# Kernel tuning notes

Measured on AMD Instinct MI355X. Metric: run time of the kernel, lower is better.

The kernel has to match this reference:

```python
import jax, jax.numpy as jnp
import numpy as np
from math import sqrt

BS, SEQ, NV, DM, K = 16, 1024, 512, 256, 8
EPS = 0.05  # sinkhorn epsilon
TEMP = 0.07  # concrete-bernoulli temperature


def setup_inputs() -> dict:
    key = jax.random.key(0)
    k1, k2, k3 = jax.random.split(key, 3)
    x = jax.random.normal(k1, (BS, SEQ, NV), jnp.float32)
    # nn.Linear(seq_len, d_model): weight [d_model, seq_len], bias [d_model]
    W = jax.random.normal(k2, (DM, SEQ), jnp.float32) / sqrt(SEQ)
    b = jnp.zeros((DM,), jnp.float32)
    cluster_emb = jax.random.normal(k3, (K, DM), jnp.float32) / sqrt(DM)
    return {"x": x, "W": W, "b": b, "cluster_emb": cluster_emb}


def _l2norm(z):
    # F.normalize(x, dim=1, p=2) with eps=1e-12 clamp
    n = jnp.maximum(jnp.linalg.norm(z, axis=1, keepdims=True), 1e-12)
    return z / n


def _sinkhorn(q):
    Q = jnp.exp(q / EPS)
    return Q / jnp.sum(Q, axis=1, keepdims=True)


def _concrete_bern(p, key):
    u = jax.random.uniform(key, p.shape, p.dtype, 1e-10, 1.0 - 1e-10)
    noise = jnp.log(u) - jnp.log1p(-u)
    logit = jnp.log(p + 1e-10) - jnp.log(1.0 - p + 1e-10)
    return jax.nn.sigmoid((logit + noise) / TEMP)


def _forward(x, W, b, cluster_emb):
    bs, S, nv = x.shape
    d = W.shape[0]
    k = cluster_emb.shape[0]
    # permute -> [bs, nv, S], Linear(S -> d)
    x_emb = jnp.einsum('bsv,ds->bvd', x, W) + b  # [bs, nv, d]
    x_flat = x_emb.reshape(-1, d)  # [bs*nv, d]
    # cosine-similarity cluster logits
    prob = (_l2norm(x_flat) @ _l2norm(cluster_emb).T).reshape(bs, nv, k)
    prob_temp = _sinkhorn(prob.reshape(-1, k)).reshape(bs, nv, k)  # individual probs
    prob_avg = _sinkhorn(jnp.mean(prob, axis=0))  # [nv, k]
    mask = _concrete_bern(prob_avg, jax.random.key(42))  # [nv, k]
    # CrossAttention with n_heads=1 (dropout inactive in eval)
    scale = 1.0 / sqrt(d)
    scores = jnp.einsum('kd,bvd->bkv', cluster_emb, x_emb)  # [bs, k, nv]
    A = jax.nn.softmax(scale * scores, axis=-1) * mask.T[None]  # masked attn
    V = jnp.einsum('bkv,bvd->bkd', A, x_emb)  # [bs, k, d]
    cluster_emb_avg = jnp.mean(V, axis=0)  # [k, d] (stored attribute in torch)
    # cluster_base_encoding: straight-through bernoulli, broadcast over seq_len
    soft = prob_temp.transpose(2, 0, 1)[..., None]  # [k, bs, nv, 1]
    u = jax.random.uniform(jax.random.key(7), soft.shape, soft.dtype)
    bern = (u < jax.lax.stop_gradient(soft)).astype(soft.dtype)
    extend = jnp.broadcast_to(bern, (k, bs, nv, S))  # [k, bs, nv, S]
    hard = soft + jax.lax.stop_gradient(extend - soft)  # straight-through
    return hard


def reference(x, W, b, cluster_emb):
    return _forward(x, W, b, cluster_emb)
```

## Files before the change

kernel.cpp:

```cpp
#include <hip/hip_runtime.h>
#include <math.h>
#include <stdint.h>

#define BS 16
#define SEQ 1024
#define NV 512
#define DM 256
#define NK 8

__device__ double g_WC[NK * SEQ];
__device__ double g_Bk[NK];
__device__ __align__(16) float g_Wt[SEQ * DM];
__device__ __align__(16) float g_zp[4 * BS * NV * DM];
__device__ double g_nn2[BS * NV];
__device__ double g_Dp[8 * BS * NV * NK];
__device__ unsigned char g_bits[BS * NV];

__device__ __forceinline__ void threefry2x32_key7(uint32_t x0, uint32_t x1,
                                                  uint32_t& o0, uint32_t& o1) {
    const uint32_t k0 = 0u, k1 = 7u;
    const uint32_t k2 = k0 ^ k1 ^ 0x1BD11BDAu;
    uint32_t v0 = x0 + k0, v1 = x1 + k1;
#define TF_ROUND(r) { v0 += v1; v1 = (v1 << (r)) | (v1 >> (32 - (r))); v1 ^= v0; }
    TF_ROUND(13) TF_ROUND(15) TF_ROUND(26) TF_ROUND(6)
    v0 += k1; v1 += k2 + 1u;
    TF_ROUND(17) TF_ROUND(29) TF_ROUND(16) TF_ROUND(24)
    v0 += k2; v1 += k0 + 2u;
    TF_ROUND(13) TF_ROUND(15) TF_ROUND(26) TF_ROUND(6)
    v0 += k0; v1 += k1 + 3u;
    TF_ROUND(17) TF_ROUND(29) TF_ROUND(16) TF_ROUND(24)
    v0 += k1; v1 += k2 + 4u;
    TF_ROUND(13) TF_ROUND(15) TF_ROUND(26) TF_ROUND(6)
    v0 += k2; v1 += k0 + 5u;
#undef TF_ROUND
    o0 = v0; o1 = v1;
}

__device__ __forceinline__ float bits_to_uniform(uint32_t b) {
    return __uint_as_float((b >> 9) | 0x3F800000u) - 1.0f;
}

__device__ __forceinline__ void cp16(const float* g, float* l) {
    __builtin_amdgcn_global_load_lds(
        (const __attribute__((address_space(1))) void*)g,
        (__attribute__((address_space(3))) void*)l,
        16, 0, 0);
}

__global__ __launch_bounds__(256) void prep_merged_kernel(
        const float* __restrict__ W, const float* __restrict__ bias,
        const float* __restrict__ ce) {
    __shared__ float tile[64][132];
    __shared__ double red[256];
    __shared__ double cen[256];
    const int t = threadIdx.x;
    const int bid = blockIdx.x;

    if (bid < 32) {
        const int s0 = (bid & 15) * 64;
        const int d0 = (bid >> 4) * 128;
#pragma unroll
        for (int p = 0; p < 32; ++p) {
            int lin = p * 256 + t;
            int d = lin >> 6, s = lin & 63;
            tile[s][d] = W[(size_t)(d0 + d) * SEQ + s0 + s];
        }
        __syncthreads();
#pragma unroll
        for (int p = 0; p < 32; ++p) {
            int lin = p * 256 + t;
            int s = lin >> 7, d = lin & 127;
            g_Wt[(size_t)(s0 + s) * DM + d0 + d] = tile[s][d];
        }
        return;
    }

    const int pid = bid - 32;
    const int k = pid >> 2;
    const int schunk = pid & 3;

    double c = (double)ce[k * DM + t];
    red[t] = c * c;
    __syncthreads();
    for (int off = 128; off > 0; off >>= 1) {
        if (t < off) red[t] += red[t + off];
        __syncthreads();
    }
    double nc = fmax(sqrt(red[0]), 1e-12);
    cen[t] = c / nc;
    __syncthreads();
    red[t] = (double)bias[t] * cen[t];
    __syncthreads();
    for (int off = 128; off > 0; off >>= 1) {
        if (t < off) red[t] += red[t + off];
        __syncthreads();
    }
    if (t == 0 && schunk == 0) g_Bk[k] = red[0];

    const int s = schunk * 256 + t;
    double acc = 0.0;
#pragma unroll 8
    for (int d = 0; d < DM; ++d)
        acc += cen[d] * (double)W[(size_t)d * SEQ + s];
    g_WC[(size_t)k * SEQ + s] = acc;
}

#define KC 16

__global__ __launch_bounds__(256) void gemm_kernel(
        const float* __restrict__ x) {
    __shared__ __align__(16) float xs[2][KC * 64];
    __shared__ __align__(16) float wst[2][KC * 256];

    const int t = threadIdx.x;
    const int kblk = blockIdx.x;
    const int vblk = blockIdx.y;
    const int b    = blockIdx.z;
    const int v0 = vblk * 64;
    const float* xb = x + (size_t)b * SEQ * NV + v0;

    const int tv8 = (t & 7) * 8;
    const int td8 = (t >> 3) * 8;
    const int w = t >> 6;
    const int l = t & 63;

    const int wrow0 = w * 4;
    const size_t g_w_lane = (size_t)l * 4;
    const int xrow_sub = l >> 4;
    const int xcol = (l & 15) * 4;

    float acc[8][8];
#pragma unroll
    for (int j = 0; j < 8; ++j)
#pragma unroll
        for (int i = 0; i < 8; ++i) acc[j][i] = 0.0f;

#define STAGE(BUF, S0)                                                         \
    {                                                                          \
        _Pragma("unroll")                                                      \
        for (int j = 0; j < 4; ++j) {                                          \
            int row = wrow0 + j;                                               \
            cp16(&g_Wt[(size_t)((S0) + row) * DM + g_w_lane],                  \
                 &wst[BUF][row * 256]);                                        \
        }                                                                      \
        cp16(&xb[(size_t)((S0) + wrow0 + xrow_sub) * NV + xcol],               \
             &xs[BUF][wrow0 * 64]);                                            \
    }

    const int sbeg = kblk * 256;

    STAGE(0, sbeg)
    __syncthreads();

    for (int c = 0; c < 16; ++c) {
        const int buf = c & 1;
        if (c < 15) STAGE(buf ^ 1, sbeg + (c + 1) * KC)

#pragma unroll
        for (int kk = 0; kk < KC; ++kk) {
            const float* xr = &xs[buf][kk * 64 + tv8];
            const float* wr = &wst[buf][kk * 256 + td8];
            float4 xv0 = *(const float4*)(xr);
            float4 xv1 = *(const float4*)(xr + 4);
            float4 wv0 = *(const float4*)(wr);
            float4 wv1 = *(const float4*)(wr + 4);
            float xv[8] = {xv0.x, xv0.y, xv0.z, xv0.w, xv1.x, xv1.y, xv1.z, xv1.w};
            float wv[8] = {wv0.x, wv0.y, wv0.z, wv0.w, wv1.x, wv1.y, wv1.z, wv1.w};
#pragma unroll
            for (int j = 0; j < 8; ++j)
#pragma unroll
                for (int i = 0; i < 8; ++i) acc[j][i] += xv[j] * wv[i];
        }

        __syncthreads();
    }
#undef STAGE

#pragma unroll
    for (int j = 0; j < 8; ++j) {
        size_t base = (size_t)kblk * (BS * NV * DM) +
                      ((size_t)b * NV + v0 + tv8 + j) * DM + td8;
#pragma unroll
        for (int m = 0; m < 8; m += 4)
            *(float4*)&g_zp[base + m] =
                make_float4(acc[j][m], acc[j][m + 1], acc[j][m + 2], acc[j][m + 3]);
    }
}

__global__ __launch_bounds__(256) void combine_kernel(
        const float* __restrict__ bias) {
    __shared__ double red[16][17];
    const int t = threadIdx.x;
    const int vg = blockIdx.x;
    const int b  = blockIdx.y;
    const int vl = t >> 4, dg = t & 15;
    const int v = vg * 16 + vl;

    const size_t bvbase = ((size_t)b * NV + v) * DM + dg * 16;
    double sq = 0.0;
#pragma unroll
    for (int m = 0; m < 16; m += 4) {
        float4 p0 = *(const float4*)&g_zp[(size_t)0 * (BS * NV * DM) + bvbase + m];
        float4 p1 = *(const float4*)&g_zp[(size_t)1 * (BS * NV * DM) + bvbase + m];
        float4 p2 = *(const float4*)&g_zp[(size_t)2 * (BS * NV * DM) + bvbase + m];
        float4 p3 = *(const float4*)&g_zp[(size_t)3 * (BS * NV * DM) + bvbase + m];
        float4 bb = *(const float4*)&bias[dg * 16 + m];
        double z0 = (double)p0.x + (double)p1.x + (double)p2.x + (double)p3.x + (double)bb.x;
        double z1 = (double)p0.y + (double)p1.y + (double)p2.y + (double)p3.y + (double)bb.y;
        double z2 = (double)p0.z + (double)p1.z + (double)p2.z + (double)p3.z + (double)bb.z;
        double z3 = (double)p0.w + (double)p1.w + (double)p2.w + (double)p3.w + (double)bb.w;
        sq += z0 * z0 + z1 * z1 + z2 * z2 + z3 * z3;
    }
    red[vl][dg] = sq;
    __syncthreads();
    if (dg == 0) {
        double s = 0.0;
#pragma unroll
        for (int i = 0; i < 16; ++i) s += red[vl][i];
        g_nn2[b * NV + v] = s;
    }
}

__global__ __launch_bounds__(256) void dkern(const float* __restrict__ x) {
    __shared__ double wcd[NK][128];
    __shared__ double dw[4][64][NK];
    const int t = threadIdx.x;
    const int vblk = blockIdx.x;
    const int b    = blockIdx.y;
    const int sc   = blockIdx.z;
    const int v0 = vblk * 64;
    const int ss = sc * 128;

#pragma unroll
    for (int j = 0; j < 4; ++j) {
        int idx = j * 256 + t;
        ((double*)wcd)[idx] = g_WC[(size_t)(idx >> 7) * SEQ + ss + (idx & 127)];
    }
    __syncthreads();

    const int vl = t & 63, w = t >> 6;
    const float* xp = x + (size_t)b * SEQ * NV + v0 + vl;
    double D[NK];
#pragma unroll
    for (int k = 0; k < NK; ++k) D[k] = 0.0;
    const int sw = w * 32;
    for (int i = 0; i < 32; ++i) {
        int sl = sw + i;
        double xv = (double)xp[(size_t)(ss + sl) * NV];
#pragma unroll
        for (int k = 0; k < NK; ++k) D[k] += xv * wcd[k][sl];
    }
#pragma unroll
    for (int k = 0; k < NK; ++k) dw[w][vl][k] = D[k];
    __syncthreads();

    const int v = t & 63, k2 = (t >> 6) * 2;
#pragma unroll
    for (int j = 0; j < 2; ++j) {
        int k = k2 + j;
        double s = dw[0][v][k] + dw[1][v][k] + dw[2][v][k] + dw[3][v][k];
        g_Dp[(((size_t)sc * BS + b) * NV + v0 + v) * NK + k] = s;
    }
}

__global__ __launch_bounds__(256) void finalize_kernel() {
    const int bv = blockIdx.x * 256 + threadIdx.x;
    double n = fmax(sqrt(g_nn2[bv]), 1e-12);

    double D[NK];
#pragma unroll
    for (int k = 0; k < NK; ++k) D[k] = g_Bk[k];
#pragma unroll
    for (int sc = 0; sc < 8; ++sc) {
#pragma unroll
        for (int k = 0; k < NK; ++k)
            D[k] += g_Dp[((size_t)sc * (BS * NV) + bv) * NK + k];
    }

    double p[NK], sum = 0.0;
#pragma unroll
    for (int k = 0; k < NK; ++k) {
        p[k] = exp((D[k] / n) / 0.05);
        sum += p[k];
    }
    unsigned int byte = 0;
#pragma unroll
    for (int k = 0; k < NK; ++k) {
        uint32_t i = (uint32_t)(k * (BS * NV) + bv);
        uint32_t y0, y1;
        threefry2x32_key7(0u, i, y0, y1);
        float u = bits_to_uniform(y0 ^ y1);
        if ((double)u < p[k] / sum) byte |= 1u << k;
    }
    g_bits[bv] = (unsigned char)byte;
}

__global__ __launch_bounds__(256) void write_kernel(float* __restrict__ out) {
    const int t = threadIdx.x;
    const size_t r0 = (size_t)blockIdx.x * 8;
#pragma unroll
    for (int j = 0; j < 8; ++j) {
        size_t r = r0 + j;
        unsigned int bv = (unsigned int)(r & 8191u);
        unsigned int k  = (unsigned int)(r >> 13);
        float v = ((g_bits[bv] >> k) & 1u) ? 1.0f : 0.0f;
        float4 val = make_float4(v, v, v, v);
        ((float4*)(out + r * 1024))[t] = val;
    }
}

extern "C" void kernel_launch(void* const* d_in, const int* in_sizes, int n_in,
                              void* d_out, int out_size, void* d_ws, size_t ws_size,
                              hipStream_t stream) {
    const float* x    = (const float*)d_in[0];
    const float* W    = (const float*)d_in[1];
    const float* bias = (const float*)d_in[2];
    const float* ce   = (const float*)d_in[3];
    float* out = (float*)d_out;

    prep_merged_kernel<<<dim3(64), dim3(256), 0, stream>>>(W, bias, ce);
    gemm_kernel<<<dim3(4, 8, 16), dim3(256), 0, stream>>>(x);
    combine_kernel<<<dim3(32, 16), dim3(256), 0, stream>>>(bias);
    dkern<<<dim3(8, 16, 8), dim3(256), 0, stream>>>(x);
    finalize_kernel<<<dim3(32), dim3(256), 0, stream>>>();
    write_kernel<<<dim3(8192), dim3(256), 0, stream>>>(out);
}
```

Before: 387.0 us.

## Read x directly from global in GEMM, double K-chunk, merge combine and dkern

The GEMM kernel stops staging the x tile in shared memory and has each thread load its x values straight from global memory, while the W tile chunk grows from 16 to 32 rows so there are half as many chunk iterations and barriers. The norm-combine kernel and the D-projection kernel are merged into one launch, with the block index picking which role each block plays, which removes one kernel launch and lets the two run side by side. The cost is uncached-looking global loads inside the inner FMA loop, where threads sharing the same x columns fetch redundantly, plus more shared memory per GEMM block.

```diff
diff --git a/kernel.cpp b/kernel.cpp
--- a/kernel.cpp
+++ b/kernel.cpp
@@ -105,11 +105,10 @@
     g_WC[(size_t)k * SEQ + s] = acc;
 }
 
-#define KC 16
+#define KC 32
 
 __global__ __launch_bounds__(256) void gemm_kernel(
         const float* __restrict__ x) {
-    __shared__ __align__(16) float xs[2][KC * 64];
     __shared__ __align__(16) float wst[2][KC * 256];
 
     const int t = threadIdx.x;
@@ -124,10 +123,8 @@
     const int w = t >> 6;
     const int l = t & 63;
 
-    const int wrow0 = w * 4;
-    const size_t g_w_lane = (size_t)l * 4;
-    const int xrow_sub = l >> 4;
-    const int xcol = (l & 15) * 4;
+    const int wrow0 = w * 8;
+    const size_t g_lane4 = (size_t)l * 4;
 
     float acc[8][8];
 #pragma unroll
@@ -138,13 +135,11 @@
 #define STAGE(BUF, S0)                                                         \
     {                                                                          \
         _Pragma("unroll")                                                      \
-        for (int j = 0; j < 4; ++j) {                                          \
+        for (int j = 0; j < 8; ++j) {                                          \
             int row = wrow0 + j;                                               \
-            cp16(&g_Wt[(size_t)((S0) + row) * DM + g_w_lane],                  \
+            cp16(&g_Wt[(size_t)((S0) + row) * DM + g_lane4],                   \
                  &wst[BUF][row * 256]);                                        \
         }                                                                      \
-        cp16(&xb[(size_t)((S0) + wrow0 + xrow_sub) * NV + xcol],               \
-             &xs[BUF][wrow0 * 64]);                                            \
     }
 
     const int sbeg = kblk * 256;
@@ -152,16 +147,16 @@
     STAGE(0, sbeg)
     __syncthreads();
 
-    for (int c = 0; c < 16; ++c) {
+    for (int c = 0; c < 8; ++c) {
         const int buf = c & 1;
-        if (c < 15) STAGE(buf ^ 1, sbeg + (c + 1) * KC)
-
+        if (c < 7) STAGE(buf ^ 1, sbeg + (c + 1) * KC)
+
+        const float* xrow = &xb[(size_t)(sbeg + c * KC) * NV + tv8];
 #pragma unroll
         for (int kk = 0; kk < KC; ++kk) {
-            const float* xr = &xs[buf][kk * 64 + tv8];
             const float* wr = &wst[buf][kk * 256 + td8];
-            float4 xv0 = *(const float4*)(xr);
-            float4 xv1 = *(const float4*)(xr + 4);
+            float4 xv0 = *(const float4*)(xrow);
+            float4 xv1 = *(const float4*)(xrow + 4);
             float4 wv0 = *(const float4*)(wr);
             float4 wv1 = *(const float4*)(wr + 4);
             float xv[8] = {xv0.x, xv0.y, xv0.z, xv0.w, xv1.x, xv1.y, xv1.z, xv1.w};
@@ -170,6 +165,7 @@
             for (int j = 0; j < 8; ++j)
 #pragma unroll
                 for (int i = 0; i < 8; ++i) acc[j][i] += xv[j] * wv[i];
+            xrow += NV;
         }
 
         __syncthreads();
@@ -187,54 +183,58 @@
     }
 }
 
-__global__ __launch_bounds__(256) void combine_kernel(
-        const float* __restrict__ bias) {
-    __shared__ double red[16][17];
+__global__ __launch_bounds__(256) void cd_kernel(
+        const float* __restrict__ bias, const float* __restrict__ x) {
+    __shared__ double sm[3072];
     const int t = threadIdx.x;
-    const int vg = blockIdx.x;
-    const int b  = blockIdx.y;
-    const int vl = t >> 4, dg = t & 15;
-    const int v = vg * 16 + vl;
-
-    const size_t bvbase = ((size_t)b * NV + v) * DM + dg * 16;
-    double sq = 0.0;
-#pragma unroll
-    for (int m = 0; m < 16; m += 4) {
-        float4 p0 = *(const float4*)&g_zp[(size_t)0 * (BS * NV * DM) + bvbase + m];
-        float4 p1 = *(const float4*)&g_zp[(size_t)1 * (BS * NV * DM) + bvbase + m];
-        float4 p2 = *(const float4*)&g_zp[(size_t)2 * (BS * NV * DM) + bvbase + m];
-        float4 p3 = *(const float4*)&g_zp[(size_t)3 * (BS * NV * DM) + bvbase + m];
-        float4 bb = *(const float4*)&bias[dg * 16 + m];
-        double z0 = (double)p0.x + (double)p1.x + (double)p2.x + (double)p3.x + (double)bb.x;
-        double z1 = (double)p0.y + (double)p1.y + (double)p2.y + (double)p3.y + (double)bb.y;
-        double z2 = (double)p0.z + (double)p1.z + (double)p2.z + (double)p3.z + (double)bb.z;
-        double z3 = (double)p0.w + (double)p1.w + (double)p2.w + (double)p3.w + (double)bb.w;
-        sq += z0 * z0 + z1 * z1 + z2 * z2 + z3 * z3;
-    }
-    red[vl][dg] = sq;
-    __syncthreads();
-    if (dg == 0) {
-        double s = 0.0;
-#pragma unroll
-        for (int i = 0; i < 16; ++i) s += red[vl][i];
-        g_nn2[b * NV + v] = s;
-    }
-}
-
-__global__ __launch_bounds__(256) void dkern(const float* __restrict__ x) {
-    __shared__ double wcd[NK][128];
-    __shared__ double dw[4][64][NK];
-    const int t = threadIdx.x;
-    const int vblk = blockIdx.x;
-    const int b    = blockIdx.y;
-    const int sc   = blockIdx.z;
+    const int bid = blockIdx.x;
+
+    if (bid < 512) {
+        const int vg = bid >> 4;
+        const int b  = bid & 15;
+        const int vl = t >> 4, dg = t & 15;
+        const int v = vg * 16 + vl;
+
+        const size_t bvbase = ((size_t)b * NV + v) * DM + dg * 16;
+        double sq = 0.0;
+#pragma unroll
+        for (int m = 0; m < 16; m += 4) {
+            float4 p0 = *(const float4*)&g_zp[(size_t)0 * (BS * NV * DM) + bvbase + m];
+            float4 p1 = *(const float4*)&g_zp[(size_t)1 * (BS * NV * DM) + bvbase + m];
+            float4 p2 = *(const float4*)&g_zp[(size_t)2 * (BS * NV * DM) + bvbase + m];
+            float4 p3 = *(const float4*)&g_zp[(size_t)3 * (BS * NV * DM) + bvbase + m];
+            float4 bb = *(const float4*)&bias[dg * 16 + m];
+            double z0 = (double)p0.x + (double)p1.x + (double)p2.x + (double)p3.x + (double)bb.x;
+            double z1 = (double)p0.y + (double)p1.y + (double)p2.y + (double)p3.y + (double)bb.y;
+            double z2 = (double)p0.z + (double)p1.z + (double)p2.z + (double)p3.z + (double)bb.z;
+            double z3 = (double)p0.w + (double)p1.w + (double)p2.w + (double)p3.w + (double)bb.w;
+            sq += z0 * z0 + z1 * z1 + z2 * z2 + z3 * z3;
+        }
+        sm[vl * 17 + dg] = sq;
+        __syncthreads();
+        if (dg == 0) {
+            double s = 0.0;
+#pragma unroll
+            for (int i = 0; i < 16; ++i) s += sm[vl * 17 + i];
+            g_nn2[b * NV + v] = s;
+        }
+        return;
+    }
+
+    const int did  = bid - 512;
+    const int vblk = did & 7;
+    const int b    = (did >> 3) & 15;
+    const int sc   = did >> 7;
     const int v0 = vblk * 64;
     const int ss = sc * 128;
 
+    double* wcd = sm;
+    double* dw  = sm + 1024;
+
 #pragma unroll
     for (int j = 0; j < 4; ++j) {
         int idx = j * 256 + t;
-        ((double*)wcd)[idx] = g_WC[(size_t)(idx >> 7) * SEQ + ss + (idx & 127)];
+        wcd[idx] = g_WC[(size_t)(idx >> 7) * SEQ + ss + (idx & 127)];
     }
     __syncthreads();
 
@@ -248,17 +248,18 @@
         int sl = sw + i;
         double xv = (double)xp[(size_t)(ss + sl) * NV];
 #pragma unroll
-        for (int k = 0; k < NK; ++k) D[k] += xv * wcd[k][sl];
-    }
-#pragma unroll
-    for (int k = 0; k < NK; ++k) dw[w][vl][k] = D[k];
+        for (int k = 0; k < NK; ++k) D[k] += xv * wcd[k * 128 + sl];
+    }
+#pragma unroll
+    for (int k = 0; k < NK; ++k) dw[(w * 64 + vl) * NK + k] = D[k];
     __syncthreads();
 
     const int v = t & 63, k2 = (t >> 6) * 2;
 #pragma unroll
     for (int j = 0; j < 2; ++j) {
         int k = k2 + j;
-        double s = dw[0][v][k] + dw[1][v][k] + dw[2][v][k] + dw[3][v][k];
+        double s = dw[(0 * 64 + v) * NK + k] + dw[(1 * 64 + v) * NK + k] +
+                   dw[(2 * 64 + v) * NK + k] + dw[(3 * 64 + v) * NK + k];
         g_Dp[(((size_t)sc * BS + b) * NV + v0 + v) * NK + k] = s;
     }
 }
@@ -320,8 +321,7 @@
 
     prep_merged_kernel<<<dim3(64), dim3(256), 0, stream>>>(W, bias, ce);
     gemm_kernel<<<dim3(4, 8, 16), dim3(256), 0, stream>>>(x);
-    combine_kernel<<<dim3(32, 16), dim3(256), 0, stream>>>(bias);
-    dkern<<<dim3(8, 16, 8), dim3(256), 0, stream>>>(x);
+    cd_kernel<<<dim3(1536), dim3(256), 0, stream>>>(bias, x);
     finalize_kernel<<<dim3(32), dim3(256), 0, stream>>>();
     write_kernel<<<dim3(8192), dim3(256), 0, stream>>>(out);
 }
```

Result: slower. 419.2 us (+8.3%).
